# Kernel tuning notes

Hardware: AMD Instinct MI355X
Metric: run time of the kernel (lower is better)

## Reference

```python
import jax, jax.numpy as jnp
import numpy as np

B, T, C, H = 512, 256, 128, 128


def setup_inputs() -> dict:
    key = jax.random.key(0)
    kx, kk, kq, kv = jax.random.split(key, 4)
    x = jax.random.normal(kx, (B, T, C), dtype=jnp.float32)
    # weights stored as [in, out]; Linear(bias=False) is x @ W
    Wk = jax.random.normal(kk, (C, H), dtype=jnp.float32) * 0.02
    Wq = jax.random.normal(kq, (C, H), dtype=jnp.float32) * 0.02
    Wv = jax.random.normal(kv, (C, H), dtype=jnp.float32) * 0.02
    return {"x": x, "Wk": Wk, "Wq": Wq, "Wv": Wv}


def reference(x, Wk, Wq, Wv):
    Bx, Tx, Cx = x.shape
    k = jnp.einsum("btc,ch->bth", x, Wk)
    q = jnp.einsum("btc,ch->bth", x, Wq)
    v = jnp.einsum("btc,ch->bth", x, Wv)
    scale = Cx ** -0.5  # NOTE: original scales by n_embd (C), not head_size
    wei = jnp.einsum("bth,bsh->bts", q, k) * scale  # [B, T, T]
    causal = jnp.tril(jnp.ones((Tx, Tx), dtype=bool))
    wei = jnp.where(causal[None, :, :], wei, -jnp.inf)
    wei = jax.nn.softmax(wei, axis=-1)
    # dropout is identity in eval mode
    out = jnp.einsum("bts,bsh->bth", wei, v)  # [B, T, H]
    return (out, k, v)  # matches (out, present=(k, v))
```

## Files before the change

kernel.cpp:

```cpp
#include <hip/hip_runtime.h>

typedef unsigned short u16;
typedef __attribute__((ext_vector_type(8))) short short8;
typedef __attribute__((ext_vector_type(4))) float float4v;

#define BTH (512*256*128)
#define MASKV (-30000.0f)

__device__ __forceinline__ u16 f2bf(float f){
    union{float f; unsigned i;} v; v.f = f;
    unsigned x = v.i;
    unsigned r = (x + 0x7FFFu + ((x >> 16) & 1u)) >> 16;
    return (u16)r;
}

__global__ void wt_kernel(const float* __restrict__ Wq, const float* __restrict__ Wk,
                          const float* __restrict__ Wv, u16* __restrict__ WT){
    int idx = blockIdx.x * 256 + threadIdx.x;
    int w   = idx >> 14;
    int rem = idx & 16383;
    int n = rem >> 7;
    int k = rem & 127;
    const float* src = (w == 0) ? Wq : (w == 1) ? Wk : Wv;
    float val = src[k * 128 + n];
    if (w == 0) val *= 0.08838834764831845f;
    WT[idx] = f2bf(val);
}

__global__ __launch_bounds__(1024, 4) void fused_kernel(const float* __restrict__ x,
                                                        const u16* __restrict__ WT,
                                                        float* __restrict__ dout){
    __shared__ u16 Kbuf [4 * 256 * 32];
    __shared__ u16 VTbuf[8 * 128 * 32];
    __shared__ u16 ps   [16 * 1024];

    int b = blockIdx.x;
    int tid = threadIdx.x;
    int w = tid >> 6, lane = tid & 63, lq = lane & 15, quad = lane >> 4;

    const int TILE[16] = {0,15,7,8, 14,1,9,6, 2,13,5,10, 12,3,11,4};
    int rg = TILE[w];

    const float* xb   = x    + (size_t)b * 256 * 128;
    float*       oout = dout + (size_t)b * 256 * 128;
    float*       kout = dout + (size_t)BTH     + (size_t)b * 256 * 128;
    float*       vout = dout + (size_t)2 * BTH + (size_t)b * 256 * 128;

    short8 ax[4];
    #pragma unroll
    for (int ks = 0; ks < 4; ks++){
        const float* px = xb + (size_t)(rg*16 + lq)*128 + ks*32 + quad*8;
        float4v lo = *(const float4v*)px;
        float4v hi = *(const float4v*)(px + 4);
        short8 s;
        #pragma unroll
        for (int j = 0; j < 4; j++){
            s[j]     = (short)f2bf(lo[j]);
            s[j + 4] = (short)f2bf(hi[j]);
        }
        ax[ks] = s;
    }

    u16* qs = Kbuf + w * 2048;
    short8 qf[4];
    {
        #pragma unroll
        for (int ht = 0; ht < 8; ht++){
            short8 bw[4];
            #pragma unroll
            for (int ks = 0; ks < 4; ks++)
                bw[ks] = *(const short8*)(WT + (size_t)(ht*16 + lq)*128 + ks*32 + quad*8);
            float4v c = {0.f,0.f,0.f,0.f};
            #pragma unroll
            for (int ks = 0; ks < 4; ks++)
                c = __builtin_amdgcn_mfma_f32_16x16x32_bf16(ax[ks], bw[ks], c, 0, 0, 0);
            #pragma unroll
            for (int r = 0; r < 4; r++)
                qs[(quad*4 + r)*128 + ht*16 + lq] = f2bf(c[r]);
        }
        #pragma unroll
        for (int ks = 0; ks < 4; ks++)
            qf[ks] = *(const short8*)(qs + lq*128 + ks*32 + quad*8);
    }
    __syncthreads();

    #pragma unroll
    for (int ht = 0; ht < 8; ht++){
        short8 bw[4];
        #pragma unroll
        for (int ks = 0; ks < 4; ks++)
            bw[ks] = *(const short8*)(WT + (size_t)16384 + (size_t)(ht*16 + lq)*128 + ks*32 + quad*8);
        float4v c = {0.f,0.f,0.f,0.f};
        #pragma unroll
        for (int ks = 0; ks < 4; ks++)
            c = __builtin_amdgcn_mfma_f32_16x16x32_bf16(ax[ks], bw[ks], c, 0, 0, 0);
        #pragma unroll
        for (int r = 0; r < 4; r++){
            int key = rg*16 + quad*4 + r;
            kout[(size_t)key*128 + ht*16 + lq] = c[r];
            Kbuf[(ht>>1)*8192 + key*32 + (ht&1)*16 + lq] = f2bf(c[r]);
        }
    }

    #pragma unroll
    for (int ht = 0; ht < 8; ht++){
        short8 bv[4];
        #pragma unroll
        for (int ks = 0; ks < 4; ks++)
            bv[ks] = *(const short8*)(WT + (size_t)2*16384 + (size_t)(ht*16 + lq)*128 + ks*32 + quad*8);
        float4v c = {0.f,0.f,0.f,0.f};
        #pragma unroll
        for (int ks = 0; ks < 4; ks++)
            c = __builtin_amdgcn_mfma_f32_16x16x32_bf16(ax[ks], bv[ks], c, 0, 0, 0);
        #pragma unroll
        for (int r = 0; r < 4; r++)
            vout[(size_t)(rg*16 + quad*4 + r)*128 + ht*16 + lq] = c[r];
        float4v ct = {0.f,0.f,0.f,0.f};
        #pragma unroll
        for (int ks = 0; ks < 4; ks++)
            ct = __builtin_amdgcn_mfma_f32_16x16x32_bf16(bv[ks], ax[ks], ct, 0, 0, 0);
        int t = rg*16 + lq;
        int e0 = (t>>5)*4096 + (t&31);
        #pragma unroll
        for (int r = 0; r < 4; r++)
            VTbuf[e0 + (ht*16 + quad*4 + r)*32] = f2bf(ct[r]);
    }
    __syncthreads();

    float4v oacc[8];
    float mrun[4], lrun[4];
    #pragma unroll
    for (int o = 0; o < 8; o++) oacc[o] = (float4v){0.f,0.f,0.f,0.f};
    #pragma unroll
    for (int r = 0; r < 4; r++){ mrun[r] = MASKV; lrun[r] = 0.f; }
    u16* psw = ps + w * 1024;

    #pragma unroll
    for (int kb = 0; kb < 4; kb++){
        if (kb*4 > rg) continue;

        float4v s4[4];
        #pragma unroll
        for (int kt2 = 0; kt2 < 4; kt2++){
            int kt = kb*4 + kt2;
            float4v c = {MASKV, MASKV, MASKV, MASKV};
            if (kt <= rg){
                c = (float4v){0.f,0.f,0.f,0.f};
                #pragma unroll
                for (int ks = 0; ks < 4; ks++){
                    short8 bb = *(const short8*)(Kbuf + ks*8192 + (kt*16 + lq)*32 + quad*8);
                    c = __builtin_amdgcn_mfma_f32_16x16x32_bf16(qf[ks], bb, c, 0, 0, 0);
                }
                #pragma unroll
                for (int r = 0; r < 4; r++)
                    c[r] = fminf(fmaxf(c[r], MASKV), 30000.0f);
                if (kt == rg){
                    #pragma unroll
                    for (int r = 0; r < 4; r++)
                        if (kt*16 + lq > rg*16 + quad*4 + r) c[r] = MASKV;
                }
            }
            s4[kt2] = c;
        }
        #pragma unroll
        for (int r = 0; r < 4; r++){
            float mx = fmaxf(fmaxf(s4[0][r], s4[1][r]), fmaxf(s4[2][r], s4[3][r]));
            mx = fmaxf(mx, __shfl_xor(mx, 1));
            mx = fmaxf(mx, __shfl_xor(mx, 2));
            mx = fmaxf(mx, __shfl_xor(mx, 4));
            mx = fmaxf(mx, __shfl_xor(mx, 8));
            float mnew = fmaxf(mrun[r], mx);
            float alpha = __expf(mrun[r] - mnew);
            float rs = 0.f;
            #pragma unroll
            for (int kt2 = 0; kt2 < 4; kt2++){
                float pv = __expf(s4[kt2][r] - mnew);
                s4[kt2][r] = pv;
                rs += pv;
            }
            rs += __shfl_xor(rs, 1);
            rs += __shfl_xor(rs, 2);
            rs += __shfl_xor(rs, 4);
            rs += __shfl_xor(rs, 8);
            lrun[r] = lrun[r] * alpha + rs;
            mrun[r] = mnew;
            #pragma unroll
            for (int o = 0; o < 8; o++) oacc[o][r] *= alpha;
        }
        #pragma unroll
        for (int kt2 = 0; kt2 < 4; kt2++)
            #pragma unroll
            for (int r = 0; r < 4; r++)
                psw[(quad*4 + r)*64 + kt2*16 + lq] = f2bf(s4[kt2][r]);
        short8 pa0 = *(const short8*)(psw + lq*64 + quad*8);
        short8 pa1 = *(const short8*)(psw + lq*64 + 32 + quad*8);
        #pragma unroll
        for (int k2 = 0; k2 < 2; k2++){
            short8 pa = (k2 == 0) ? pa0 : pa1;
            #pragma unroll
            for (int o = 0; o < 8; o++){
                short8 vb = *(const short8*)(VTbuf + (kb*2 + k2)*4096 + (o*16 + lq)*32 + quad*8);
                oacc[o] = __builtin_amdgcn_mfma_f32_16x16x32_bf16(pa, vb, oacc[o], 0, 0, 0);
            }
        }
    }

    #pragma unroll
    for (int r = 0; r < 4; r++){
        float inv = 1.0f / lrun[r];
        int row = rg*16 + quad*4 + r;
        #pragma unroll
        for (int o = 0; o < 8; o++)
            oout[(size_t)row*128 + o*16 + lq] = oacc[o][r] * inv;
    }
}

extern "C" void kernel_launch(void* const* d_in, const int* in_sizes, int n_in,
                              void* d_out, int out_size, void* d_ws, size_t ws_size,
                              hipStream_t stream){
    const float* x  = (const float*)d_in[0];
    const float* Wk = (const float*)d_in[1];
    const float* Wq = (const float*)d_in[2];
    const float* Wv = (const float*)d_in[3];
    float* out = (float*)d_out;
    u16* WT = (u16*)d_ws;

    wt_kernel   <<<192,  256, 0, stream>>>(Wq, Wk, Wv, WT);
    fused_kernel<<<512, 1024, 0, stream>>>(x, WT, out);
}
```

Measured before the change: 323.0 us.

## Split each batch across two 512-thread blocks by query half

Each batch is now handled by two blocks of 8 waves instead of one 1024-thread block. The upper-half block recomputes K and V for the lower 128 keys in a second phase rather than sharing them, which halves shared memory per block and doubles the grid. The aim is better occupancy and scheduling granularity. The cost is redundant K/V projection work for the upper half and an extra barrier between phases.

```diff
diff --git a/kernel.cpp b/kernel.cpp
--- a/kernel.cpp
+++ b/kernel.cpp
@@ -27,43 +27,41 @@
     WT[idx] = f2bf(val);
 }
 
-__global__ __launch_bounds__(1024, 4) void fused_kernel(const float* __restrict__ x,
-                                                        const u16* __restrict__ WT,
-                                                        float* __restrict__ dout){
-    __shared__ u16 Kbuf [4 * 256 * 32];
-    __shared__ u16 VTbuf[8 * 128 * 32];
-    __shared__ u16 ps   [16 * 1024];
-
-    int b = blockIdx.x;
+__global__ __launch_bounds__(512, 4) void fused_kernel(const float* __restrict__ x,
+                                                       const u16* __restrict__ WT,
+                                                       float* __restrict__ dout){
+    __shared__ u16 Kbuf [4 * 128 * 32];
+    __shared__ u16 VTbuf[4 * 128 * 32];
+    __shared__ u16 ps   [8 * 1024];
+
+    int lb = blockIdx.x;
+    int b = lb >> 1, hi = lb & 1;
+    int r0 = hi << 7;
     int tid = threadIdx.x;
     int w = tid >> 6, lane = tid & 63, lq = lane & 15, quad = lane >> 4;
 
-    const int TILE[16] = {0,15,7,8, 14,1,9,6, 2,13,5,10, 12,3,11,4};
-    int rg = TILE[w];
+    const int TILE8[8] = {0,7,3,4, 6,1,5,2};
+    int lt = TILE8[w];
 
     const float* xb   = x    + (size_t)b * 256 * 128;
     float*       oout = dout + (size_t)b * 256 * 128;
     float*       kout = dout + (size_t)BTH     + (size_t)b * 256 * 128;
     float*       vout = dout + (size_t)2 * BTH + (size_t)b * 256 * 128;
 
-    short8 ax[4];
-    #pragma unroll
-    for (int ks = 0; ks < 4; ks++){
-        const float* px = xb + (size_t)(rg*16 + lq)*128 + ks*32 + quad*8;
-        float4v lo = *(const float4v*)px;
-        float4v hi = *(const float4v*)(px + 4);
-        short8 s;
-        #pragma unroll
-        for (int j = 0; j < 4; j++){
-            s[j]     = (short)f2bf(lo[j]);
-            s[j + 4] = (short)f2bf(hi[j]);
-        }
-        ax[ks] = s;
-    }
-
-    u16* qs = Kbuf + w * 2048;
     short8 qf[4];
     {
+        short8 axq[4];
+        #pragma unroll
+        for (int ks = 0; ks < 4; ks++){
+            const float* px = xb + (size_t)(r0 + lt*16 + lq)*128 + ks*32 + quad*8;
+            float4v lo = *(const float4v*)px;
+            float4v hiv = *(const float4v*)(px + 4);
+            short8 s;
+            #pragma unroll
+            for (int j = 0; j < 4; j++){ s[j] = (short)f2bf(lo[j]); s[j+4] = (short)f2bf(hiv[j]); }
+            axq[ks] = s;
+        }
+        u16* qs = Kbuf + w * 2048;
         #pragma unroll
         for (int ht = 0; ht < 8; ht++){
             short8 bw[4];
@@ -73,7 +71,7 @@
             float4v c = {0.f,0.f,0.f,0.f};
             #pragma unroll
             for (int ks = 0; ks < 4; ks++)
-                c = __builtin_amdgcn_mfma_f32_16x16x32_bf16(ax[ks], bw[ks], c, 0, 0, 0);
+                c = __builtin_amdgcn_mfma_f32_16x16x32_bf16(axq[ks], bw[ks], c, 0, 0, 0);
             #pragma unroll
             for (int r = 0; r < 4; r++)
                 qs[(quad*4 + r)*128 + ht*16 + lq] = f2bf(c[r]);
@@ -81,49 +79,6 @@
         #pragma unroll
         for (int ks = 0; ks < 4; ks++)
             qf[ks] = *(const short8*)(qs + lq*128 + ks*32 + quad*8);
-    }
-    __syncthreads();
-
-    #pragma unroll
-    for (int ht = 0; ht < 8; ht++){
-        short8 bw[4];
-        #pragma unroll
-        for (int ks = 0; ks < 4; ks++)
-            bw[ks] = *(const short8*)(WT + (size_t)16384 + (size_t)(ht*16 + lq)*128 + ks*32 + quad*8);
-        float4v c = {0.f,0.f,0.f,0.f};
-        #pragma unroll
-        for (int ks = 0; ks < 4; ks++)
-            c = __builtin_amdgcn_mfma_f32_16x16x32_bf16(ax[ks], bw[ks], c, 0, 0, 0);
-        #pragma unroll
-        for (int r = 0; r < 4; r++){
-            int key = rg*16 + quad*4 + r;
-            kout[(size_t)key*128 + ht*16 + lq] = c[r];
-            Kbuf[(ht>>1)*8192 + key*32 + (ht&1)*16 + lq] = f2bf(c[r]);
-        }
-    }
-
-    #pragma unroll
-    for (int ht = 0; ht < 8; ht++){
-        short8 bv[4];
-        #pragma unroll
-        for (int ks = 0; ks < 4; ks++)
-            bv[ks] = *(const short8*)(WT + (size_t)2*16384 + (size_t)(ht*16 + lq)*128 + ks*32 + quad*8);
-        float4v c = {0.f,0.f,0.f,0.f};
-        #pragma unroll
-        for (int ks = 0; ks < 4; ks++)
-            c = __builtin_amdgcn_mfma_f32_16x16x32_bf16(ax[ks], bv[ks], c, 0, 0, 0);
-        #pragma unroll
-        for (int r = 0; r < 4; r++)
-            vout[(size_t)(rg*16 + quad*4 + r)*128 + ht*16 + lq] = c[r];
-        float4v ct = {0.f,0.f,0.f,0.f};
-        #pragma unroll
-        for (int ks = 0; ks < 4; ks++)
-            ct = __builtin_amdgcn_mfma_f32_16x16x32_bf16(bv[ks], ax[ks], ct, 0, 0, 0);
-        int t = rg*16 + lq;
-        int e0 = (t>>5)*4096 + (t&31);
-        #pragma unroll
-        for (int r = 0; r < 4; r++)
-            VTbuf[e0 + (ht*16 + quad*4 + r)*32] = f2bf(ct[r]);
     }
     __syncthreads();
 
@@ -135,80 +90,141 @@
     for (int r = 0; r < 4; r++){ mrun[r] = MASKV; lrun[r] = 0.f; }
     u16* psw = ps + w * 1024;
 
-    #pragma unroll
-    for (int kb = 0; kb < 4; kb++){
-        if (kb*4 > rg) continue;
-
-        float4v s4[4];
-        #pragma unroll
-        for (int kt2 = 0; kt2 < 4; kt2++){
-            int kt = kb*4 + kt2;
-            float4v c = {MASKV, MASKV, MASKV, MASKV};
-            if (kt <= rg){
-                c = (float4v){0.f,0.f,0.f,0.f};
-                #pragma unroll
-                for (int ks = 0; ks < 4; ks++){
-                    short8 bb = *(const short8*)(Kbuf + ks*8192 + (kt*16 + lq)*32 + quad*8);
-                    c = __builtin_amdgcn_mfma_f32_16x16x32_bf16(qf[ks], bb, c, 0, 0, 0);
-                }
+    for (int p = 0; p <= hi; p++){
+        bool own = (p == hi);
+        int srcr0 = own ? r0 : 0;
+
+        short8 axp[4];
+        #pragma unroll
+        for (int ks = 0; ks < 4; ks++){
+            const float* px = xb + (size_t)(srcr0 + lt*16 + lq)*128 + ks*32 + quad*8;
+            float4v lo = *(const float4v*)px;
+            float4v hiv = *(const float4v*)(px + 4);
+            short8 s;
+            #pragma unroll
+            for (int j = 0; j < 4; j++){ s[j] = (short)f2bf(lo[j]); s[j+4] = (short)f2bf(hiv[j]); }
+            axp[ks] = s;
+        }
+
+        #pragma unroll
+        for (int ht = 0; ht < 8; ht++){
+            short8 bw[4];
+            #pragma unroll
+            for (int ks = 0; ks < 4; ks++)
+                bw[ks] = *(const short8*)(WT + (size_t)16384 + (size_t)(ht*16 + lq)*128 + ks*32 + quad*8);
+            float4v c = {0.f,0.f,0.f,0.f};
+            #pragma unroll
+            for (int ks = 0; ks < 4; ks++)
+                c = __builtin_amdgcn_mfma_f32_16x16x32_bf16(axp[ks], bw[ks], c, 0, 0, 0);
+            #pragma unroll
+            for (int r = 0; r < 4; r++){
+                int keyl = lt*16 + quad*4 + r;
+                if (own) kout[(size_t)(srcr0 + keyl)*128 + ht*16 + lq] = c[r];
+                Kbuf[(ht>>1)*4096 + keyl*32 + (ht&1)*16 + lq] = f2bf(c[r]);
+            }
+        }
+        #pragma unroll
+        for (int ht = 0; ht < 8; ht++){
+            short8 bv[4];
+            #pragma unroll
+            for (int ks = 0; ks < 4; ks++)
+                bv[ks] = *(const short8*)(WT + (size_t)2*16384 + (size_t)(ht*16 + lq)*128 + ks*32 + quad*8);
+            if (own){
+                float4v c = {0.f,0.f,0.f,0.f};
+                #pragma unroll
+                for (int ks = 0; ks < 4; ks++)
+                    c = __builtin_amdgcn_mfma_f32_16x16x32_bf16(axp[ks], bv[ks], c, 0, 0, 0);
                 #pragma unroll
                 for (int r = 0; r < 4; r++)
-                    c[r] = fminf(fmaxf(c[r], MASKV), 30000.0f);
-                if (kt == rg){
+                    vout[(size_t)(srcr0 + lt*16 + quad*4 + r)*128 + ht*16 + lq] = c[r];
+            }
+            float4v ct = {0.f,0.f,0.f,0.f};
+            #pragma unroll
+            for (int ks = 0; ks < 4; ks++)
+                ct = __builtin_amdgcn_mfma_f32_16x16x32_bf16(bv[ks], axp[ks], ct, 0, 0, 0);
+            int tl = lt*16 + lq;
+            #pragma unroll
+            for (int r = 0; r < 4; r++)
+                VTbuf[(tl>>5)*4096 + (ht*16 + quad*4 + r)*32 + (tl&31)] = f2bf(ct[r]);
+        }
+        __syncthreads();
+
+        #pragma unroll
+        for (int kbL = 0; kbL < 2; kbL++){
+            if (own && kbL*4 > lt) continue;
+
+            float4v s4[4];
+            #pragma unroll
+            for (int kt2 = 0; kt2 < 4; kt2++){
+                int kt = kbL*4 + kt2;
+                float4v c = {MASKV, MASKV, MASKV, MASKV};
+                if (!own || kt <= lt){
+                    c = (float4v){0.f,0.f,0.f,0.f};
+                    #pragma unroll
+                    for (int ks = 0; ks < 4; ks++){
+                        short8 bb = *(const short8*)(Kbuf + ks*4096 + (kt*16 + lq)*32 + quad*8);
+                        c = __builtin_amdgcn_mfma_f32_16x16x32_bf16(qf[ks], bb, c, 0, 0, 0);
+                    }
                     #pragma unroll
                     for (int r = 0; r < 4; r++)
-                        if (kt*16 + lq > rg*16 + quad*4 + r) c[r] = MASKV;
+                        c[r] = fminf(fmaxf(c[r], MASKV), 30000.0f);
+                    if (own && kt == lt){
+                        #pragma unroll
+                        for (int r = 0; r < 4; r++)
+                            if (lq > quad*4 + r) c[r] = MASKV;
+                    }
                 }
-            }
-            s4[kt2] = c;
-        }
-        #pragma unroll
-        for (int r = 0; r < 4; r++){
-            float mx = fmaxf(fmaxf(s4[0][r], s4[1][r]), fmaxf(s4[2][r], s4[3][r]));
-            mx = fmaxf(mx, __shfl_xor(mx, 1));
-            mx = fmaxf(mx, __shfl_xor(mx, 2));
-            mx = fmaxf(mx, __shfl_xor(mx, 4));
-            mx = fmaxf(mx, __shfl_xor(mx, 8));
-            float mnew = fmaxf(mrun[r], mx);
-            float alpha = __expf(mrun[r] - mnew);
-            float rs = 0.f;
-            #pragma unroll
-            for (int kt2 = 0; kt2 < 4; kt2++){
-                float pv = __expf(s4[kt2][r] - mnew);
-                s4[kt2][r] = pv;
-                rs += pv;
-            }
-            rs += __shfl_xor(rs, 1);
-            rs += __shfl_xor(rs, 2);
-            rs += __shfl_xor(rs, 4);
-            rs += __shfl_xor(rs, 8);
-            lrun[r] = lrun[r] * alpha + rs;
-            mrun[r] = mnew;
-            #pragma unroll
-            for (int o = 0; o < 8; o++) oacc[o][r] *= alpha;
-        }
-        #pragma unroll
-        for (int kt2 = 0; kt2 < 4; kt2++)
-            #pragma unroll
-            for (int r = 0; r < 4; r++)
-                psw[(quad*4 + r)*64 + kt2*16 + lq] = f2bf(s4[kt2][r]);
-        short8 pa0 = *(const short8*)(psw + lq*64 + quad*8);
-        short8 pa1 = *(const short8*)(psw + lq*64 + 32 + quad*8);
-        #pragma unroll
-        for (int k2 = 0; k2 < 2; k2++){
-            short8 pa = (k2 == 0) ? pa0 : pa1;
-            #pragma unroll
-            for (int o = 0; o < 8; o++){
-                short8 vb = *(const short8*)(VTbuf + (kb*2 + k2)*4096 + (o*16 + lq)*32 + quad*8);
-                oacc[o] = __builtin_amdgcn_mfma_f32_16x16x32_bf16(pa, vb, oacc[o], 0, 0, 0);
-            }
-        }
+                s4[kt2] = c;
+            }
+            #pragma unroll
+            for (int r = 0; r < 4; r++){
+                float mx = fmaxf(fmaxf(s4[0][r], s4[1][r]), fmaxf(s4[2][r], s4[3][r]));
+                mx = fmaxf(mx, __shfl_xor(mx, 1));
+                mx = fmaxf(mx, __shfl_xor(mx, 2));
+                mx = fmaxf(mx, __shfl_xor(mx, 4));
+                mx = fmaxf(mx, __shfl_xor(mx, 8));
+                float mnew = fmaxf(mrun[r], mx);
+                float alpha = __expf(mrun[r] - mnew);
+                float rs = 0.f;
+                #pragma unroll
+                for (int kt2 = 0; kt2 < 4; kt2++){
+                    float pv = __expf(s4[kt2][r] - mnew);
+                    s4[kt2][r] = pv;
+                    rs += pv;
+                }
+                rs += __shfl_xor(rs, 1);
+                rs += __shfl_xor(rs, 2);
+                rs += __shfl_xor(rs, 4);
+                rs += __shfl_xor(rs, 8);
+                lrun[r] = lrun[r] * alpha + rs;
+                mrun[r] = mnew;
+                #pragma unroll
+                for (int o = 0; o < 8; o++) oacc[o][r] *= alpha;
+            }
+            #pragma unroll
+            for (int kt2 = 0; kt2 < 4; kt2++)
+                #pragma unroll
+                for (int r = 0; r < 4; r++)
+                    psw[(quad*4 + r)*64 + kt2*16 + lq] = f2bf(s4[kt2][r]);
+            short8 pa0 = *(const short8*)(psw + lq*64 + quad*8);
+            short8 pa1 = *(const short8*)(psw + lq*64 + 32 + quad*8);
+            #pragma unroll
+            for (int k2 = 0; k2 < 2; k2++){
+                short8 pa = (k2 == 0) ? pa0 : pa1;
+                #pragma unroll
+                for (int o = 0; o < 8; o++){
+                    short8 vb = *(const short8*)(VTbuf + (kbL*2 + k2)*4096 + (o*16 + lq)*32 + quad*8);
+                    oacc[o] = __builtin_amdgcn_mfma_f32_16x16x32_bf16(pa, vb, oacc[o], 0, 0, 0);
+                }
+            }
+        }
+        if (p < hi) __syncthreads();
     }
 
     #pragma unroll
     for (int r = 0; r < 4; r++){
         float inv = 1.0f / lrun[r];
-        int row = rg*16 + quad*4 + r;
+        int row = r0 + lt*16 + quad*4 + r;
         #pragma unroll
         for (int o = 0; o < 8; o++)
             oout[(size_t)row*128 + o*16 + lq] = oacc[o][r] * inv;
@@ -226,5 +242,5 @@
     u16* WT = (u16*)d_ws;
 
     wt_kernel   <<<192,  256, 0, stream>>>(Wq, Wk, Wv, WT);
-    fused_kernel<<<512, 1024, 0, stream>>>(x, WT, out);
-}
+    fused_kernel<<<1024, 512, 0, stream>>>(x, WT, out);
+}
```

Result: slower. 671.7 us (+108.0%).
